# Optimization experiments

Measured on AMD Instinct MI355X. Metric: run time of the kernel, lower is better.

Reference implementation:

```python
import jax, jax.numpy as jnp
import numpy as np

EMA_OLD = 0.01  # original: m[z] = m[z]*0.01 + y*0.99
EMA_NEW = 0.99

def setup_inputs() -> dict:
    key = jax.random.key(0)
    k1, k2, k3, k4 = jax.random.split(key, 4)
    B, n, C, L = 4096, 1024, 64, 64
    y = jax.random.normal(k1, (B, C, L), dtype=jnp.float32)   # encoder latents
    m = jax.random.normal(k2, (n, C, L), dtype=jnp.float32)   # codebook means
    sd = jax.random.uniform(k3, (n, C, L), dtype=jnp.float32) # codebook variances (init ones in orig)
    p = jax.random.uniform(k4, (n,), dtype=jnp.float32)       # cluster counts
    return {"y": y, "m": m, "sd": sd, "p": p}

def reference(y, m, sd, p):
    B, C, L = y.shape
    n = m.shape[0]
    # pairwise squared distances via ||y||^2 - 2 y.m + ||m||^2 (GEMM form)
    yf = y.reshape(B, C * L)
    mf = m.reshape(n, C * L)
    d2 = ((yf * yf).sum(-1, keepdims=True)
          - 2.0 * (yf @ mf.T)
          + (mf * mf).sum(-1)[None, :])            # [B, n]
    z = jnp.argmin(d2, axis=1)                      # [B] assignments
    new_m = m.at[z].set(m[z] * EMA_OLD + y * EMA_NEW)
    # original updates sd using the ALREADY-updated m gathered at z
    mg = new_m[z]
    new_sd = sd.at[z].set((mg - y) ** 2 * EMA_OLD + sd[z] * EMA_NEW)
    return jnp.concatenate([new_m, new_sd], axis=0)  # [2n, C, L]
```

## Files before the change

kernel.cpp:

```cpp
#include <hip/hip_runtime.h>

#define B_ROWS 4096
#define N_CLUST 1024
#define KDIM 4096
#define NKT 32
#define NSTEP 32

#define EMA_OLD 0.01f
#define EMA_NEW 0.99f
#define MARGIN 2.0f
#define PSCALE 16.0f
#define PLANE ((size_t)B_ROWS * N_CLUST)

typedef unsigned short ushortT;
typedef _Float16 half8 __attribute__((ext_vector_type(8)));
typedef short short8v __attribute__((ext_vector_type(8)));
typedef float f32x16 __attribute__((ext_vector_type(16)));

#define WS_WINNER_OFF 0
#define WS_YY_OFF     20480
#define WS_MM_OFF     36864
#define WS_P_OFF      65536
#define WS_YHI_OFF    (WS_P_OFF + 33554432)
#define WS_MHI_OFF    (WS_YHI_OFF + 33554432)
#define WS_END        (WS_MHI_OFF + 8388608)

__global__ __launch_bounds__(256) void convert_sumsq(
    const float* __restrict__ ysrc, const float* __restrict__ msrc,
    ushortT* __restrict__ yhi, ushortT* __restrict__ mhi,
    float* __restrict__ yy, float* __restrict__ mm,
    int* __restrict__ winner) {
    const int blk = blockIdx.x;
    const float* src;
    ushortT* hi;
    float* out;
    int row;
    if (blk < B_ROWS) {
        src = ysrc; hi = yhi; out = yy + blk; row = blk;
    } else {
        row = blk - B_ROWS;
        src = msrc; hi = mhi; out = mm + row;
        if (threadIdx.x == 0) winner[row] = -1;
    }
    const int r = row & 63, rb = row >> 6;
    const int t = threadIdx.x;
    float s = 0.f;
#pragma unroll
    for (int h = 0; h < 2; ++h) {
        int ci = h * 256 + t;
        int kt = ci >> 4, p = ci & 15;
        int c = p ^ (r & 15);
        const float* sp = src + ((size_t)row << 12) + kt * 128 + c * 8;
        float4 v0 = *(const float4*)sp;
        float4 v1 = *(const float4*)(sp + 4);
        float vv[8] = {v0.x, v0.y, v0.z, v0.w, v1.x, v1.y, v1.z, v1.w};
        half8 hv;
#pragma unroll
        for (int i = 0; i < 8; ++i) {
            hv[i] = (_Float16)vv[i];
            s += vv[i] * vv[i];
        }
        size_t off = (((size_t)rb * NKT + kt) * 64 + r) * 128 + p * 8;
        *(half8*)(hi + off) = hv;
    }
    for (int off = 32; off > 0; off >>= 1) s += __shfl_down(s, off, 64);
    __shared__ float red[4];
    if ((t & 63) == 0) red[t >> 6] = s;
    __syncthreads();
    if (t == 0) out[0] = red[0] + red[1] + red[2] + red[3];
}

__device__ __forceinline__ void gload_lds16(const void* g, void* l) {
    __builtin_amdgcn_global_load_lds(
        (const __attribute__((address_space(1))) unsigned int*)g,
        (__attribute__((address_space(3))) unsigned int*)l, 16, 0, 0);
}

__device__ __forceinline__ half8 ldfrag_pair(const ushortT* s, int r, int c) {
    int q = r >> 1;
    int sl = ((((r & 1) << 3) | c) ^ (q & 15));
    return *(const half8*)(s + q * 128 + sl * 8);
}

__global__ __launch_bounds__(256, 2) void screen_gemm(
    const ushortT* __restrict__ Ah, const ushortT* __restrict__ Bh,
    short* __restrict__ pws) {
    __shared__ __align__(16) ushortT sA[2][128 * 64];
    __shared__ __align__(16) ushortT sB[2][128 * 64];

    const int t = threadIdx.x, w = t >> 6, l = t & 63;
    const int by = blockIdx.x & 7;
    const int kh = (blockIdx.x >> 3) & 1;
    const int bx = blockIdx.x >> 4;
    const int row0 = bx * 128, col0 = by * 128;
    const int wr = (w >> 1) * 64, wc = (w & 1) * 64;
    const int m0 = l & 31, hsel = l >> 5;

    int laneoff[4];
#pragma unroll
    for (int j = 0; j < 4; ++j) {
        int g = w * 4 + j;
        int q = g * 4 + (l >> 4);
        int u = (l & 15) ^ (q & 15);
        int rr = 2 * q + (u >> 3);
        int R = rr & 63;
        int hi3 = (R >> 3) & 1;
        laneoff[j] = R * 256 + ((((hi3 << 3) | ((u & 7) ^ (R & 7)))) << 4);
    }

    f32x16 acc[2][2];
#pragma unroll
    for (int i = 0; i < 2; ++i)
#pragma unroll
        for (int j = 0; j < 2; ++j)
#pragma unroll
            for (int r = 0; r < 16; ++r) acc[i][j][r] = 0.f;

    const int ra0 = wr + m0, ra1 = wr + 32 + m0;
    const int rb0 = wc + m0, rb1 = wc + 32 + m0;

#define STAGE(buf, step)                                                      \
    {                                                                         \
        const int kt_ = kh * (NKT / 2) + ((step) >> 1);                       \
        const int ks_ = (step) & 1;                                           \
        _Pragma("unroll")                                                     \
        for (int j = 0; j < 4; ++j) {                                         \
            const int g = w * 4 + j;                                          \
            const int lo = laneoff[j] ^ (ks_ << 7);                           \
            const size_t tbA =                                                \
                ((size_t)((2 * bx + (g >> 3)) * NKT + kt_) << 14);            \
            const size_t tbB =                                                \
                ((size_t)((2 * by + (g >> 3)) * NKT + kt_) << 14);            \
            gload_lds16((const char*)Ah + tbA + lo,                           \
                        (char*)&sA[buf][0] + g * 1024);                       \
            gload_lds16((const char*)Bh + tbB + lo,                           \
                        (char*)&sB[buf][0] + g * 1024);                       \
        }                                                                     \
    }

    STAGE(0, 0);

#pragma unroll 2
    for (int i = 0; i < NSTEP; ++i) {
        const int buf = i & 1;
        if (i + 1 < NSTEP) {
            STAGE(buf ^ 1, i + 1);
            asm volatile("s_waitcnt vmcnt(8)" ::: "memory");
        } else {
            asm volatile("s_waitcnt vmcnt(0)" ::: "memory");
        }
        __builtin_amdgcn_s_barrier();

        const ushortT* tA = &sA[buf][0];
        const ushortT* tB = &sB[buf][0];
        __builtin_amdgcn_s_setprio(1);
#pragma unroll
        for (int kk = 0; kk < 4; ++kk) {
            int c = kk * 2 + hsel;
            half8 a0 = ldfrag_pair(tA, ra0, c);
            half8 a1 = ldfrag_pair(tA, ra1, c);
            half8 b0 = ldfrag_pair(tB, rb0, c);
            half8 b1 = ldfrag_pair(tB, rb1, c);
            acc[0][0] = __builtin_amdgcn_mfma_f32_32x32x16_f16(a0, b0, acc[0][0], 0, 0, 0);
            acc[0][1] = __builtin_amdgcn_mfma_f32_32x32x16_f16(a0, b1, acc[0][1], 0, 0, 0);
            acc[1][0] = __builtin_amdgcn_mfma_f32_32x32x16_f16(a1, b0, acc[1][0], 0, 0, 0);
            acc[1][1] = __builtin_amdgcn_mfma_f32_32x32x16_f16(a1, b1, acc[1][1], 0, 0, 0);
        }
        __builtin_amdgcn_s_setprio(0);
        asm volatile("" ::: "memory");
        __builtin_amdgcn_s_barrier();
    }
#undef STAGE

    short* pk = pws + (size_t)kh * PLANE;
#pragma unroll
    for (int i = 0; i < 2; ++i)
#pragma unroll
        for (int j = 0; j < 2; ++j) {
            const int gcol = col0 + wc + j * 32 + m0;
#pragma unroll
            for (int r = 0; r < 16; ++r) {
                int ri = (r & 3) + 8 * (r >> 2) + 4 * hsel;
                int grow = row0 + wr + i * 32 + ri;
                float q = fmaxf(fminf(acc[i][j][r] * (-2.0f * PSCALE),
                                      32767.f), -32767.f);
                pk[(size_t)grow * N_CLUST + gcol] = (short)__float2int_rn(q);
            }
        }
}

__global__ __launch_bounds__(256) void rescreen(
    const short* __restrict__ pws, const float* __restrict__ ysrc,
    const float* __restrict__ msrc, const float* __restrict__ yy,
    const float* __restrict__ mm, int* __restrict__ winner) {
    const int row = blockIdx.x * 4 + (threadIdx.x >> 6);
    const int l = threadIdx.x & 63;
    const size_t rb = (size_t)row * N_CLUST;

    int sacc[16];
#pragma unroll
    for (int q = 0; q < 16; ++q) sacc[q] = 0;
    const short* base = pws + rb + l * 16;
#pragma unroll
    for (int pl = 0; pl < 2; ++pl) {
        const short8v* sp = (const short8v*)(base + pl * PLANE);
        short8v x0 = sp[0], x1 = sp[1];
#pragma unroll
        for (int e = 0; e < 8; ++e) {
            sacc[e] += (int)x0[e];
            sacc[8 + e] += (int)x1[e];
        }
    }
    float v[16];
    const float4* mmv = (const float4*)(mm + l * 16);
#pragma unroll
    for (int h = 0; h < 4; ++h) {
        float4 mv = mmv[h];
        v[h * 4 + 0] = mv.x + (float)sacc[h * 4 + 0] * (1.0f / PSCALE);
        v[h * 4 + 1] = mv.y + (float)sacc[h * 4 + 1] * (1.0f / PSCALE);
        v[h * 4 + 2] = mv.z + (float)sacc[h * 4 + 2] * (1.0f / PSCALE);
        v[h * 4 + 3] = mv.w + (float)sacc[h * 4 + 3] * (1.0f / PSCALE);
    }

    float m1 = v[0], m2 = 3.0e38f;
    int a1 = l * 16;
#pragma unroll
    for (int q = 1; q < 16; ++q) {
        float x = v[q];
        if (x < m1) { m2 = m1; m1 = x; a1 = l * 16 + q; }
        else m2 = fminf(m2, x);
    }
#pragma unroll
    for (int s = 1; s <= 32; s <<= 1) {
        float o1 = __shfl_xor(m1, s, 64);
        int ob = __shfl_xor(a1, s, 64);
        float o2 = __shfl_xor(m2, s, 64);
        if (o1 < m1 || (o1 == m1 && ob < a1)) {
            m2 = fminf(o2, m1); m1 = o1; a1 = ob;
        } else {
            m2 = fminf(m2, o1);
        }
    }

    int zj;
    if (m2 - m1 > MARGIN) {
        zj = a1;
    } else {
        const float thr = m1 + MARGIN;
        double bestd = 1e300;
        int bestj = 0x7FFFFFFF;
        const float yyr = yy[row];
        const float4* yp = (const float4*)(ysrc + (size_t)row * KDIM);
        for (int q = 0; q < 16; ++q) {
            unsigned long long mask = __ballot(v[q] <= thr);
            while (mask) {
                int lb = __ffsll((unsigned long long)mask) - 1;
                mask &= mask - 1;
                int j = lb * 16 + q;
                const float4* mp = (const float4*)(msrc + (size_t)j * KDIM);
                double acc = 0.0;
#pragma unroll
                for (int tt = 0; tt < 16; ++tt) {
                    float4 a = yp[l + 64 * tt];
                    float4 b = mp[l + 64 * tt];
                    acc += (double)a.x * b.x + (double)a.y * b.y +
                           (double)a.z * b.z + (double)a.w * b.w;
                }
#pragma unroll
                for (int s = 1; s <= 32; s <<= 1)
                    acc += __shfl_xor(acc, s, 64);
                double d2x = (double)yyr - 2.0 * acc + (double)mm[j];
                if (d2x < bestd || (d2x == bestd && j < bestj)) {
                    bestd = d2x; bestj = j;
                }
            }
        }
        zj = bestj;
    }
    if (l == 0) atomicMax(&winner[zj], row);
}

__global__ __launch_bounds__(256) void write_out(
    const float* __restrict__ y, const float* __restrict__ m,
    const float* __restrict__ sd, const int* __restrict__ winner,
    float* __restrict__ out) {
    const int idx = blockIdx.x;
    const int t = threadIdx.x;
    const int w = winner[idx];
    const float4* mp = (const float4*)(m + (size_t)idx * KDIM);
    const float4* sp = (const float4*)(sd + (size_t)idx * KDIM);
    float4* om = (float4*)(out + (size_t)idx * KDIM);
    float4* os = (float4*)(out + (size_t)(N_CLUST + idx) * KDIM);
    if (w >= 0) {
        const float4* yp = (const float4*)(y + (size_t)w * KDIM);
        for (int i = t; i < KDIM / 4; i += 256) {
            float4 mv = mp[i], yv = yp[i], sv = sp[i];
            float4 nm, ns;
            nm.x = mv.x * EMA_OLD + yv.x * EMA_NEW;
            nm.y = mv.y * EMA_OLD + yv.y * EMA_NEW;
            nm.z = mv.z * EMA_OLD + yv.z * EMA_NEW;
            nm.w = mv.w * EMA_OLD + yv.w * EMA_NEW;
            float dx = nm.x - yv.x, dy = nm.y - yv.y;
            float dz = nm.z - yv.z, dw = nm.w - yv.w;
            ns.x = dx * dx * EMA_OLD + sv.x * EMA_NEW;
            ns.y = dy * dy * EMA_OLD + sv.y * EMA_NEW;
            ns.z = dz * dz * EMA_OLD + sv.z * EMA_NEW;
            ns.w = dw * dw * EMA_OLD + sv.w * EMA_NEW;
            om[i] = nm;
            os[i] = ns;
        }
    } else {
        for (int i = t; i < KDIM / 4; i += 256) {
            om[i] = mp[i];
            os[i] = sp[i];
        }
    }
}

extern "C" void kernel_launch(void* const* d_in, const int* in_sizes, int n_in,
                              void* d_out, int out_size, void* d_ws,
                              size_t ws_size, hipStream_t stream) {
    const float* y  = (const float*)d_in[0];
    const float* m  = (const float*)d_in[1];
    const float* sd = (const float*)d_in[2];
    float* out = (float*)d_out;

    char* ws = (char*)d_ws;
    int* winner = (int*)(ws + WS_WINNER_OFF);
    float* yy   = (float*)(ws + WS_YY_OFF);
    float* mm   = (float*)(ws + WS_MM_OFF);
    short* pws  = (short*)(ws + WS_P_OFF);
    ushortT* yhi = (ushortT*)(ws + WS_YHI_OFF);
    ushortT* mhi = (ushortT*)(ws + WS_MHI_OFF);

    convert_sumsq<<<B_ROWS + N_CLUST, 256, 0, stream>>>(
        y, m, yhi, mhi, yy, mm, winner);

    screen_gemm<<<(B_ROWS / 128) * (N_CLUST / 128) * 2, 256, 0, stream>>>(
        yhi, mhi, pws);

    rescreen<<<B_ROWS / 4, 256, 0, stream>>>(pws, y, m, yy, mm, winner);

    write_out<<<N_CLUST, 256, 0, stream>>>(y, m, sd, winner, out);
}
```

Measured before the change: 214.1 us.

## Split screening GEMM K into four partitions with half-size LDS stages

The screening GEMM now splits K four ways instead of two, doubling the grid. Each stage loads a 32-wide K slice instead of 64, which halves LDS per block and lets launch bounds target four blocks per CU. The LDS swizzle and fragment addressing are redone for the narrower tile, and the rescreen kernel sums four partial planes. This aims for more occupancy and latency hiding, at the cost of more partial-sum plane traffic in the workspace and more barriers per unit of work.

```diff
diff --git a/kernel.cpp b/kernel.cpp
--- a/kernel.cpp
+++ b/kernel.cpp
@@ -76,36 +76,36 @@
         (__attribute__((address_space(3))) unsigned int*)l, 16, 0, 0);
 }
 
-__device__ __forceinline__ half8 ldfrag_pair(const ushortT* s, int r, int c) {
-    int q = r >> 1;
-    int sl = ((((r & 1) << 3) | c) ^ (q & 15));
+__device__ __forceinline__ half8 ldfrag32(const ushortT* s, int r, int c) {
+    int q = r >> 2;
+    int sl = ((((r & 3) << 2) | c) ^ (q & 15));
     return *(const half8*)(s + q * 128 + sl * 8);
 }
 
-__global__ __launch_bounds__(256, 2) void screen_gemm(
+__global__ __launch_bounds__(256, 4) void screen_gemm(
     const ushortT* __restrict__ Ah, const ushortT* __restrict__ Bh,
     short* __restrict__ pws) {
-    __shared__ __align__(16) ushortT sA[2][128 * 64];
-    __shared__ __align__(16) ushortT sB[2][128 * 64];
+    __shared__ __align__(16) ushortT sA[2][128 * 32];
+    __shared__ __align__(16) ushortT sB[2][128 * 32];
 
     const int t = threadIdx.x, w = t >> 6, l = t & 63;
     const int by = blockIdx.x & 7;
-    const int kh = (blockIdx.x >> 3) & 1;
-    const int bx = blockIdx.x >> 4;
+    const int kh = (blockIdx.x >> 3) & 3;
+    const int bx = blockIdx.x >> 5;
     const int row0 = bx * 128, col0 = by * 128;
     const int wr = (w >> 1) * 64, wc = (w & 1) * 64;
     const int m0 = l & 31, hsel = l >> 5;
 
-    int laneoff[4];
-#pragma unroll
-    for (int j = 0; j < 4; ++j) {
-        int g = w * 4 + j;
-        int q = g * 4 + (l >> 4);
+    int lane01[2];
+#pragma unroll
+    for (int j = 0; j < 2; ++j) {
+        int g = w * 2 + j;
+        int q = 4 * g + (l >> 4);
         int u = (l & 15) ^ (q & 15);
-        int rr = 2 * q + (u >> 3);
-        int R = rr & 63;
-        int hi3 = (R >> 3) & 1;
-        laneoff[j] = R * 256 + ((((hi3 << 3) | ((u & 7) ^ (R & 7)))) << 4);
+        int rl = 4 * q + (u >> 2);
+        int R = rl & 63;
+        int p0 = (R & 12) | ((u & 3) ^ (R & 3));
+        lane01[j] = R * 256 + (p0 << 4);
     }
 
     f32x16 acc[2][2];
@@ -121,31 +121,30 @@
 
 #define STAGE(buf, step)                                                      \
     {                                                                         \
-        const int kt_ = kh * (NKT / 2) + ((step) >> 1);                       \
-        const int ks_ = (step) & 1;                                           \
+        const int kt_ = kh * 8 + ((step) >> 2);                               \
+        const int x2_ = ((step) & 3) << 6;                                    \
         _Pragma("unroll")                                                     \
-        for (int j = 0; j < 4; ++j) {                                         \
-            const int g = w * 4 + j;                                          \
-            const int lo = laneoff[j] ^ (ks_ << 7);                           \
+        for (int j = 0; j < 2; ++j) {                                         \
+            const int g = w * 2 + j;                                          \
             const size_t tbA =                                                \
-                ((size_t)((2 * bx + (g >> 3)) * NKT + kt_) << 14);            \
+                ((size_t)((2 * bx + (g >> 2)) * NKT + kt_) << 14);            \
+            gload_lds16((const char*)Ah + tbA + (lane01[j] ^ x2_),            \
+                        (char*)&sA[buf][0] + g * 1024);                       \
             const size_t tbB =                                                \
-                ((size_t)((2 * by + (g >> 3)) * NKT + kt_) << 14);            \
-            gload_lds16((const char*)Ah + tbA + lo,                           \
-                        (char*)&sA[buf][0] + g * 1024);                       \
-            gload_lds16((const char*)Bh + tbB + lo,                           \
+                ((size_t)((2 * by + (g >> 2)) * NKT + kt_) << 14);            \
+            gload_lds16((const char*)Bh + tbB + (lane01[j] ^ x2_),            \
                         (char*)&sB[buf][0] + g * 1024);                       \
         }                                                                     \
     }
 
     STAGE(0, 0);
 
-#pragma unroll 2
+#pragma unroll 4
     for (int i = 0; i < NSTEP; ++i) {
         const int buf = i & 1;
         if (i + 1 < NSTEP) {
             STAGE(buf ^ 1, i + 1);
-            asm volatile("s_waitcnt vmcnt(8)" ::: "memory");
+            asm volatile("s_waitcnt vmcnt(4)" ::: "memory");
         } else {
             asm volatile("s_waitcnt vmcnt(0)" ::: "memory");
         }
@@ -155,12 +154,12 @@
         const ushortT* tB = &sB[buf][0];
         __builtin_amdgcn_s_setprio(1);
 #pragma unroll
-        for (int kk = 0; kk < 4; ++kk) {
+        for (int kk = 0; kk < 2; ++kk) {
             int c = kk * 2 + hsel;
-            half8 a0 = ldfrag_pair(tA, ra0, c);
-            half8 a1 = ldfrag_pair(tA, ra1, c);
-            half8 b0 = ldfrag_pair(tB, rb0, c);
-            half8 b1 = ldfrag_pair(tB, rb1, c);
+            half8 a0 = ldfrag32(tA, ra0, c);
+            half8 a1 = ldfrag32(tA, ra1, c);
+            half8 b0 = ldfrag32(tB, rb0, c);
+            half8 b1 = ldfrag32(tB, rb1, c);
             acc[0][0] = __builtin_amdgcn_mfma_f32_32x32x16_f16(a0, b0, acc[0][0], 0, 0, 0);
             acc[0][1] = __builtin_amdgcn_mfma_f32_32x32x16_f16(a0, b1, acc[0][1], 0, 0, 0);
             acc[1][0] = __builtin_amdgcn_mfma_f32_32x32x16_f16(a1, b0, acc[1][0], 0, 0, 0);
@@ -202,7 +201,7 @@
     for (int q = 0; q < 16; ++q) sacc[q] = 0;
     const short* base = pws + rb + l * 16;
 #pragma unroll
-    for (int pl = 0; pl < 2; ++pl) {
+    for (int pl = 0; pl < 4; ++pl) {
         const short8v* sp = (const short8v*)(base + pl * PLANE);
         short8v x0 = sp[0], x1 = sp[1];
 #pragma unroll
@@ -336,7 +335,7 @@
     convert_sumsq<<<B_ROWS + N_CLUST, 256, 0, stream>>>(
         y, m, yhi, mhi, yy, mm, winner);
 
-    screen_gemm<<<(B_ROWS / 128) * (N_CLUST / 128) * 2, 256, 0, stream>>>(
+    screen_gemm<<<(B_ROWS / 128) * (N_CLUST / 128) * 4, 256, 0, stream>>>(
         yhi, mhi, pws);
 
     rescreen<<<B_ROWS / 4, 256, 0, stream>>>(pws, y, m, yy, mm, winner);
```

After: 218.7 us. +2.1%, slower.
